# Kernel tuning notes

Measured on AMD Instinct MI355X. Metric: run time of the kernel, lower is better.

Reference implementation:

```python
import jax, jax.numpy as jnp
import numpy as np

EMBEDDING_DIM = 512
MODEL_DIM = EMBEDDING_DIM
B, S = 32, 2048


def setup_inputs() -> dict:
    key = jax.random.key(0)
    ks = jax.random.split(key, 9)
    d, m = EMBEDDING_DIM, MODEL_DIM
    # xavier_uniform bounds
    def xavier(k, shape):
        fan_out, fan_in = shape
        lim = jnp.sqrt(6.0 / (fan_in + fan_out))
        return jax.random.uniform(k, shape, jnp.float32, -lim, lim)
    return {
        "query": jax.random.normal(ks[0], (B, d), jnp.float32),
        "keys": jax.random.normal(ks[1], (B, S, 2 * d), jnp.float32),
        "key_padding_mask": jax.random.randint(ks[2], (B, S), 0, 2) > 0,
        "Wa_w": xavier(ks[3], (m, d)),
        "Wa_b": jnp.zeros((m,), jnp.float32),
        "Ua_w": xavier(ks[4], (m, 2 * d)),
        "Ua_b": jnp.zeros((m,), jnp.float32),
        "Va_w": xavier(ks[5], (1, m)),
        "Va_b": jnp.zeros((1,), jnp.float32),
    }


def reference(query, keys, key_padding_mask, Wa_w, Wa_b, Ua_w, Ua_b, Va_w, Va_b):
    # Wa(query): [B, M]; Ua(keys): [B, S, M]
    wq = query @ Wa_w.T + Wa_b                      # [B, M]
    uk = jnp.einsum('bse,me->bsm', keys, Ua_w) + Ua_b  # [B, S, M]
    e = jnp.tanh(wq[:, None, :] + uk)               # [B, S, M]
    scores = jnp.einsum('bsm,om->bos', e, Va_w) + Va_b[None, :, None]  # [B, 1, S]
    scores = jnp.where(key_padding_mask[:, None, :], -jnp.inf, scores)
    attn = jax.nn.softmax(scores, axis=-1)          # [B, 1, S]
    context = jnp.einsum('bos,bse->boe', attn, keys)  # [B, 1, 2*EMBEDDING_DIM]
    return context
```

## Files before the change

### kernel.cpp

```cpp
#include <hip/hip_runtime.h>
#include <hip/hip_bf16.h>
#include <cstdint>
#include <cstddef>

#define B_   32
#define S_   2048
#define D_   512
#define K2D  1024
#define M_   512

#define WS_SCORES 0
#define WS_EXPS   65536
#define WS_DENOM  131072
#define WS_WQ     131104
#define WS_FLAG   147488

typedef __attribute__((ext_vector_type(8))) short bf16x8;
typedef __attribute__((ext_vector_type(4))) float f32x4;

__device__ __forceinline__ float tanh_fast(float x) {
    float e = __expf(2.0f * x);
    return 1.0f - 2.0f * __builtin_amdgcn_rcpf(e + 1.0f);
}

union Pack8 { bf16x8 v; __hip_bfloat162 h[4]; };
__device__ __forceinline__ bf16x8 cvt8(float4 a, float4 b) {
    Pack8 p;
    p.h[0] = __float22bfloat162_rn(make_float2(a.x, a.y));
    p.h[1] = __float22bfloat162_rn(make_float2(a.z, a.w));
    p.h[2] = __float22bfloat162_rn(make_float2(b.x, b.y));
    p.h[3] = __float22bfloat162_rn(make_float2(b.z, b.w));
    return p.v;
}

__global__ void k_zero(float* __restrict__ scores, float* __restrict__ denom,
                       float* __restrict__ out) {
    int tid = blockIdx.x * 256 + threadIdx.x;
    if (tid < 65536) scores[tid] = 0.f;
    else if (tid < 65568) denom[tid - 65536] = 0.f;
    if (tid < 32768) out[tid] = 0.f;
}

__global__ void k_flag(const unsigned int* __restrict__ maskw, int* __restrict__ flag) {
    __shared__ int found;
    if (threadIdx.x == 0) found = 0;
    __syncthreads();
    int f = 0;
    for (int i = 0; i < 64; ++i) {
        unsigned v = maskw[threadIdx.x * 64 + i];
        if (v > 1u) f = 1;
    }
    if (f) atomicOr(&found, 1);
    __syncthreads();
    if (threadIdx.x == 0) *flag = found;
}

__global__ __launch_bounds__(256) void k_wq(const float* __restrict__ query,
                                            const float* __restrict__ Wa_w,
                                            const float* __restrict__ Wa_b,
                                            float* __restrict__ wq) {
    int tid = blockIdx.x * 256 + threadIdx.x;
    int b = tid >> 9, m = tid & 511;
    const float4* q = (const float4*)(query + (size_t)b * D_);
    const float4* w = (const float4*)(Wa_w + (size_t)m * D_);
    float acc = 0.f;
    for (int i = 0; i < D_ / 4; ++i) {
        float4 qv = q[i], wv = w[i];
        acc = fmaf(qv.x, wv.x, acc);
        acc = fmaf(qv.y, wv.y, acc);
        acc = fmaf(qv.z, wv.z, acc);
        acc = fmaf(qv.w, wv.w, acc);
    }
    wq[tid] = acc + Wa_b[m];
}

__global__ __launch_bounds__(256, 2) void k_scores(const float* __restrict__ keys,
                                                   const float* __restrict__ Ua_w,
                                                   const float* __restrict__ Ua_b,
                                                   const float* __restrict__ Va_w,
                                                   const float* __restrict__ wq,
                                                   float* __restrict__ scores) {
    __shared__ ushort As[128 * 72];
    __shared__ ushort Bs[128 * 72];

    const int t  = threadIdx.x;
    const int m0 = blockIdx.x * 128;
    const int s0 = blockIdx.y * 128;
    const int b  = blockIdx.z;
    const int wave = t >> 6, lane = t & 63;
    const int q = lane >> 4, r = lane & 15;
    const int sw = (wave >> 1) * 64, mw = (wave & 1) * 64;
    const int rb = t >> 3;
    const int kq = t & 7;

    const float* Ab = keys + ((size_t)b * S_ + s0 + rb) * K2D + kq * 8;
    const float* Bb = Ua_w + ((size_t)(m0 + rb)) * K2D + kq * 8;
    ushort* aw = &As[rb * 72 + kq * 8];
    ushort* bw = &Bs[rb * 72 + kq * 8];

    f32x4 acc[4][4];
#pragma unroll
    for (int i = 0; i < 4; ++i)
#pragma unroll
        for (int j = 0; j < 4; ++j) acc[i][j] = (f32x4){0.f, 0.f, 0.f, 0.f};

    for (int kt = 0; kt < K2D / 64; ++kt) {
        const int ko = kt * 64;
#pragma unroll
        for (int p = 0; p < 4; ++p) {
            const float* sa = Ab + (size_t)(p * 32) * K2D + ko;
            float4 a0 = *(const float4*)sa;
            float4 a1 = *(const float4*)(sa + 4);
            *(bf16x8*)(aw + p * 32 * 72) = cvt8(a0, a1);
            const float* sb = Bb + (size_t)(p * 32) * K2D + ko;
            float4 b0 = *(const float4*)sb;
            float4 b1 = *(const float4*)(sb + 4);
            *(bf16x8*)(bw + p * 32 * 72) = cvt8(b0, b1);
        }
        __syncthreads();
#pragma unroll
        for (int ks = 0; ks < 2; ++ks) {
            bf16x8 af[4], bfr[4];
#pragma unroll
            for (int i = 0; i < 4; ++i)
                af[i] = *(const bf16x8*)&As[(sw + i * 16 + r) * 72 + ks * 32 + q * 8];
#pragma unroll
            for (int j = 0; j < 4; ++j)
                bfr[j] = *(const bf16x8*)&Bs[(mw + j * 16 + r) * 72 + ks * 32 + q * 8];
#pragma unroll
            for (int i = 0; i < 4; ++i)
#pragma unroll
                for (int j = 0; j < 4; ++j)
                    acc[i][j] = __builtin_amdgcn_mfma_f32_16x16x32_bf16(
                        af[i], bfr[j], acc[i][j], 0, 0, 0);
        }
        __syncthreads();
    }

    float vaw[4], wqb[4];
#pragma unroll
    for (int j = 0; j < 4; ++j) {
        int m = m0 + mw + 16 * j + r;
        vaw[j] = Va_w[m];
        wqb[j] = wq[b * M_ + m] + Ua_b[m];
    }
    float* red = (float*)As;
    const int col = (wave & 1) * 16 + r;
#pragma unroll
    for (int i = 0; i < 4; ++i) {
#pragma unroll
        for (int rg = 0; rg < 4; ++rg) {
            int sl = sw + 16 * i + 4 * q + rg;
            float p = 0.f;
#pragma unroll
            for (int j = 0; j < 4; ++j)
                p += vaw[j] * tanh_fast(acc[i][j][rg] + wqb[j]);
            red[sl * 33 + col] = p;
        }
    }
    __syncthreads();
    if (t < 128) {
        float sum = 0.f;
#pragma unroll
        for (int c = 0; c < 32; ++c) sum += red[t * 33 + c];
        atomicAdd(&scores[(size_t)b * S_ + s0 + t], sum);
    }
}

__global__ __launch_bounds__(256) void k_softmax(const float* __restrict__ scores,
                                                 const void* __restrict__ mask,
                                                 const int* __restrict__ flag,
                                                 float* __restrict__ exps,
                                                 float* __restrict__ denom) {
    const int b = blockIdx.x, t = threadIdx.x;
    const bool bytemode = (*flag) != 0;
    const int* mi = (const int*)mask;
    const unsigned char* mb = (const unsigned char*)mask;
    float lsum = 0.f;
#pragma unroll
    for (int i = 0; i < 8; ++i) {
        int s = i * 256 + t;
        size_t idx = (size_t)b * S_ + s;
        bool m = bytemode ? (mb[idx] != 0) : (mi[idx] != 0);
        float v = m ? 0.f : expf(scores[idx]);
        exps[idx] = v;
        lsum += v;
    }
#pragma unroll
    for (int off = 32; off > 0; off >>= 1) lsum += __shfl_down(lsum, off, 64);
    __shared__ float wsum[4];
    if ((t & 63) == 0) wsum[t >> 6] = lsum;
    __syncthreads();
    if (t == 0) denom[b] = wsum[0] + wsum[1] + wsum[2] + wsum[3];
}

__global__ __launch_bounds__(256) void k_context(const float* __restrict__ keys,
                                                 const float* __restrict__ exps,
                                                 const float* __restrict__ denom,
                                                 float* __restrict__ out) {
    __shared__ float w[64];
    const int s0 = blockIdx.x * 64;
    const int b  = blockIdx.y;
    const int t  = threadIdx.x;
    if (t < 64) w[t] = exps[(size_t)b * S_ + s0 + t];
    __syncthreads();
    const float4* kp = (const float4*)(keys + ((size_t)b * S_ + s0) * K2D);
    float4 acc = {0.f, 0.f, 0.f, 0.f};
#pragma unroll 8
    for (int s = 0; s < 64; ++s) {
        float ws = w[s];
        float4 kv = kp[(size_t)s * 256 + t];
        acc.x = fmaf(ws, kv.x, acc.x);
        acc.y = fmaf(ws, kv.y, acc.y);
        acc.z = fmaf(ws, kv.z, acc.z);
        acc.w = fmaf(ws, kv.w, acc.w);
    }
    float inv = 1.0f / denom[b];
    atomicAdd(&out[b * 1024 + t * 4 + 0], acc.x * inv);
    atomicAdd(&out[b * 1024 + t * 4 + 1], acc.y * inv);
    atomicAdd(&out[b * 1024 + t * 4 + 2], acc.z * inv);
    atomicAdd(&out[b * 1024 + t * 4 + 3], acc.w * inv);
}

extern "C" void kernel_launch(void* const* d_in, const int* in_sizes, int n_in,
                              void* d_out, int out_size, void* d_ws, size_t ws_size,
                              hipStream_t stream) {
    const float* query = (const float*)d_in[0];
    const float* keys  = (const float*)d_in[1];
    const void*  mask  = d_in[2];
    const float* Wa_w  = (const float*)d_in[3];
    const float* Wa_b  = (const float*)d_in[4];
    const float* Ua_w  = (const float*)d_in[5];
    const float* Ua_b  = (const float*)d_in[6];
    const float* Va_w  = (const float*)d_in[7];

    float* wsf    = (float*)d_ws;
    float* scores = wsf + WS_SCORES;
    float* exps   = wsf + WS_EXPS;
    float* denom  = wsf + WS_DENOM;
    float* wq     = wsf + WS_WQ;
    int*   flag   = (int*)(wsf + WS_FLAG);
    float* out    = (float*)d_out;

    k_zero<<<257, 256, 0, stream>>>(scores, denom, out);
    k_flag<<<1, 256, 0, stream>>>((const unsigned int*)mask, flag);
    k_wq<<<64, 256, 0, stream>>>(query, Wa_w, Wa_b, wq);
    k_scores<<<dim3(M_ / 128, S_ / 128, B_), 256, 0, stream>>>(keys, Ua_w, Ua_b,
                                                               Va_w, wq, scores);
    k_softmax<<<B_, 256, 0, stream>>>(scores, mask, flag, exps, denom);
    k_context<<<dim3(S_ / 64, B_), 256, 0, stream>>>(keys, exps, denom, out);
}
```

Measured before the change: 570.6 us.

## Pre-convert Ua weights to bf16, read B fragments directly, remap blocks per XCD

A new kernel converts Ua_w to bf16 once in workspace. The scores GEMM then loads B fragments straight from global or L2 instead of staging them through shared memory, which halves the LDS footprint and allows three blocks per CU. The grid becomes 1D and is remapped so that the four M-tiles sharing one keys tile run on the same XCD, improving L2 reuse of keys. The mask-flag scan is also spread over 16 blocks using a global atomic. The direct global B loads could add latency, and the fast path depends on the workspace being large enough.

```diff
diff --git a/kernel.cpp b/kernel.cpp
--- a/kernel.cpp
+++ b/kernel.cpp
@@ -14,6 +14,8 @@
 #define WS_DENOM  131072
 #define WS_WQ     131104
 #define WS_FLAG   147488
+#define WS_UAB16  147520
+#define WS_NEED_BYTES (147520 * 4 + 1048576)
 
 typedef __attribute__((ext_vector_type(8))) short bf16x8;
 typedef __attribute__((ext_vector_type(4))) float f32x4;
@@ -34,25 +36,29 @@
 }
 
 __global__ void k_zero(float* __restrict__ scores, float* __restrict__ denom,
-                       float* __restrict__ out) {
+                       float* __restrict__ out, int* __restrict__ flag) {
     int tid = blockIdx.x * 256 + threadIdx.x;
     if (tid < 65536) scores[tid] = 0.f;
     else if (tid < 65568) denom[tid - 65536] = 0.f;
     if (tid < 32768) out[tid] = 0.f;
+    if (tid == 65568) *flag = 0;
 }
 
 __global__ void k_flag(const unsigned int* __restrict__ maskw, int* __restrict__ flag) {
-    __shared__ int found;
-    if (threadIdx.x == 0) found = 0;
-    __syncthreads();
+    int base = (blockIdx.x * 256 + threadIdx.x) * 4;
     int f = 0;
-    for (int i = 0; i < 64; ++i) {
-        unsigned v = maskw[threadIdx.x * 64 + i];
-        if (v > 1u) f = 1;
-    }
-    if (f) atomicOr(&found, 1);
-    __syncthreads();
-    if (threadIdx.x == 0) *flag = found;
+#pragma unroll
+    for (int i = 0; i < 4; ++i)
+        if (maskw[base + i] > 1u) f = 1;
+    if (f) atomicOr(flag, 1);
+}
+
+__global__ __launch_bounds__(256) void k_cvtB(const float* __restrict__ Ua_w,
+                                              ushort* __restrict__ Ub16) {
+    int i = (blockIdx.x * 256 + threadIdx.x) * 8;
+    float4 a = *(const float4*)(Ua_w + i);
+    float4 b = *(const float4*)(Ua_w + i + 4);
+    *(bf16x8*)(Ub16 + i) = cvt8(a, b);
 }
 
 __global__ __launch_bounds__(256) void k_wq(const float* __restrict__ query,
@@ -74,29 +80,35 @@
     wq[tid] = acc + Wa_b[m];
 }
 
-__global__ __launch_bounds__(256, 2) void k_scores(const float* __restrict__ keys,
+template <int USEB16>
+__global__ __launch_bounds__(256, 3) void k_scores(const float* __restrict__ keys,
                                                    const float* __restrict__ Ua_w,
+                                                   const ushort* __restrict__ Ub16,
                                                    const float* __restrict__ Ua_b,
                                                    const float* __restrict__ Va_w,
                                                    const float* __restrict__ wq,
                                                    float* __restrict__ scores) {
     __shared__ ushort As[128 * 72];
-    __shared__ ushort Bs[128 * 72];
-
-    const int t  = threadIdx.x;
-    const int m0 = blockIdx.x * 128;
-    const int s0 = blockIdx.y * 128;
-    const int b  = blockIdx.z;
+
+    const int h    = blockIdx.x;
+    const int xcd  = h & 7, slot = h >> 3;
+    const int mj   = slot & 3;
+    const int grp  = xcd + 8 * (slot >> 2);
+    const int b    = grp >> 4;
+    const int s0   = (grp & 15) * 128;
+    const int m0   = mj * 128;
+
+    const int t = threadIdx.x;
     const int wave = t >> 6, lane = t & 63;
     const int q = lane >> 4, r = lane & 15;
     const int sw = (wave >> 1) * 64, mw = (wave & 1) * 64;
     const int rb = t >> 3;
     const int kq = t & 7;
 
-    const float* Ab = keys + ((size_t)b * S_ + s0 + rb) * K2D + kq * 8;
-    const float* Bb = Ua_w + ((size_t)(m0 + rb)) * K2D + kq * 8;
+    const float*  Ab   = keys + ((size_t)b * S_ + s0 + rb) * K2D + kq * 8;
+    const ushort* Bb16 = Ub16 + (size_t)(m0 + mw + r) * K2D;
+    const float*  Bb32 = Ua_w + (size_t)(m0 + mw + r) * K2D;
     ushort* aw = &As[rb * 72 + kq * 8];
-    ushort* bw = &Bs[rb * 72 + kq * 8];
 
     f32x4 acc[4][4];
 #pragma unroll
@@ -112,10 +124,6 @@
             float4 a0 = *(const float4*)sa;
             float4 a1 = *(const float4*)(sa + 4);
             *(bf16x8*)(aw + p * 32 * 72) = cvt8(a0, a1);
-            const float* sb = Bb + (size_t)(p * 32) * K2D + ko;
-            float4 b0 = *(const float4*)sb;
-            float4 b1 = *(const float4*)(sb + 4);
-            *(bf16x8*)(bw + p * 32 * 72) = cvt8(b0, b1);
         }
         __syncthreads();
 #pragma unroll
@@ -125,8 +133,16 @@
             for (int i = 0; i < 4; ++i)
                 af[i] = *(const bf16x8*)&As[(sw + i * 16 + r) * 72 + ks * 32 + q * 8];
 #pragma unroll
-            for (int j = 0; j < 4; ++j)
-                bfr[j] = *(const bf16x8*)&Bs[(mw + j * 16 + r) * 72 + ks * 32 + q * 8];
+            for (int j = 0; j < 4; ++j) {
+                const int off = j * 16 * K2D + ko + ks * 32 + q * 8;
+                if (USEB16) {
+                    bfr[j] = *(const bf16x8*)(Bb16 + off);
+                } else {
+                    float4 b0 = *(const float4*)(Bb32 + off);
+                    float4 b1 = *(const float4*)(Bb32 + off + 4);
+                    bfr[j] = cvt8(b0, b1);
+                }
+            }
 #pragma unroll
             for (int i = 0; i < 4; ++i)
 #pragma unroll
@@ -234,19 +250,26 @@
     const float* Ua_b  = (const float*)d_in[6];
     const float* Va_w  = (const float*)d_in[7];
 
-    float* wsf    = (float*)d_ws;
-    float* scores = wsf + WS_SCORES;
-    float* exps   = wsf + WS_EXPS;
-    float* denom  = wsf + WS_DENOM;
-    float* wq     = wsf + WS_WQ;
-    int*   flag   = (int*)(wsf + WS_FLAG);
-    float* out    = (float*)d_out;
-
-    k_zero<<<257, 256, 0, stream>>>(scores, denom, out);
-    k_flag<<<1, 256, 0, stream>>>((const unsigned int*)mask, flag);
+    float*  wsf    = (float*)d_ws;
+    float*  scores = wsf + WS_SCORES;
+    float*  exps   = wsf + WS_EXPS;
+    float*  denom  = wsf + WS_DENOM;
+    float*  wq     = wsf + WS_WQ;
+    int*    flag   = (int*)(wsf + WS_FLAG);
+    ushort* Ub16   = (ushort*)(wsf + WS_UAB16);
+    float*  out    = (float*)d_out;
+
+    const bool big = ws_size >= (size_t)WS_NEED_BYTES;
+
+    k_zero<<<257, 256, 0, stream>>>(scores, denom, out, flag);
+    k_flag<<<16, 256, 0, stream>>>((const unsigned int*)mask, flag);
     k_wq<<<64, 256, 0, stream>>>(query, Wa_w, Wa_b, wq);
-    k_scores<<<dim3(M_ / 128, S_ / 128, B_), 256, 0, stream>>>(keys, Ua_w, Ua_b,
-                                                               Va_w, wq, scores);
+    if (big) {
+        k_cvtB<<<256, 256, 0, stream>>>(Ua_w, Ub16);
+        k_scores<1><<<2048, 256, 0, stream>>>(keys, Ua_w, Ub16, Ua_b, Va_w, wq, scores);
+    } else {
+        k_scores<0><<<2048, 256, 0, stream>>>(keys, Ua_w, Ub16, Ua_b, Va_w, wq, scores);
+    }
     k_softmax<<<B_, 256, 0, stream>>>(scores, mask, flag, exps, denom);
     k_context<<<dim3(S_ / 64, B_), 256, 0, stream>>>(keys, exps, denom, out);
 }
```

After: 574.5 us. No clear change (+0.7%).
